# Optimization experiments

Measured on AMD Instinct MI355X. Metric: run time of the kernel, lower is better.

## Reference

```python
import jax, jax.numpy as jnp
import numpy as np

B, S, H, NH = 2, 2048, 1024, 16
HD = H // NH
BASE = 10000.0


def _rotate_half(x):
    x1, x2 = x[..., : x.shape[-1] // 2], x[..., x.shape[-1] // 2 :]
    return jnp.concatenate((-x2, x1), axis=-1)


def setup_inputs() -> dict:
    key = jax.random.key(0)
    ks = jax.random.split(key, 6)
    hidden_states = jax.random.normal(ks[0], (B, S, H), jnp.float32)
    scale = 0.02
    wq = jax.random.normal(ks[1], (H, H), jnp.float32) * scale
    wk = jax.random.normal(ks[2], (H, H), jnp.float32) * scale
    wv = jax.random.normal(ks[3], (H, H), jnp.float32) * scale
    wo = jax.random.normal(ks[4], (H, H), jnp.float32) * scale
    # additive causal mask, shape (B, 1, S, S): 0 on/below diagonal, large negative above
    neg = jnp.finfo(jnp.float32).min
    causal = jnp.where(jnp.tril(jnp.ones((S, S), dtype=bool)), 0.0, neg).astype(jnp.float32)
    attention_mask = jnp.broadcast_to(causal[None, None], (B, 1, S, S))
    position_ids = jnp.broadcast_to(jnp.arange(S, dtype=jnp.int32)[None], (B, S))
    return {
        "hidden_states": hidden_states,
        "attention_mask": attention_mask,
        "wq": wq,
        "wk": wk,
        "wv": wv,
        "wo": wo,
        "position_ids": position_ids,
    }


def reference(hidden_states, attention_mask, wq, wk, wv, wo, position_ids):
    b, s, h = hidden_states.shape
    dtype = hidden_states.dtype

    def proj(x, w):  # torch Linear: y = x @ w.T, then split heads -> (b, nh, s, hd)
        y = jnp.einsum("bsh,oh->bso", x, w)
        return y.reshape(b, s, NH, HD).transpose(0, 2, 1, 3)

    q = proj(hidden_states, wq)
    k = proj(hidden_states, wk)
    v = proj(hidden_states, wv)

    # rotary cache (computed in fp32 like torch), gathered by position_ids
    inv_freq = 1.0 / (BASE ** (jnp.arange(0, HD, 2, dtype=jnp.float32) / HD))
    t = jnp.arange(s, dtype=jnp.float32)
    freqs = jnp.outer(t, inv_freq)                  # (s, hd/2)
    emb = jnp.concatenate((freqs, freqs), axis=-1)  # (s, hd)
    pos = jnp.clip(position_ids, 0, s - 1)
    cos = jnp.cos(emb).astype(dtype)[pos][:, None]  # (b, 1, s, hd)
    sin = jnp.sin(emb).astype(dtype)[pos][:, None]

    q = q * cos + _rotate_half(q) * sin
    k = k * cos + _rotate_half(k) * sin

    scores = jnp.einsum("bhqd,bhkd->bhqk", q, k) / jnp.sqrt(jnp.asarray(HD, dtype))
    scores = scores + attention_mask
    attn = jax.nn.softmax(scores.astype(jnp.float32), axis=-1).astype(dtype)
    out = jnp.einsum("bhqk,bhkd->bhqd", attn, v)    # (b, nh, s, hd)
    out = out.transpose(0, 2, 1, 3).reshape(b, s, h)
    return jnp.einsum("bso,ho->bsh", out, wo)
```

## Files before the change

### kernel.cpp

```cpp
#include <hip/hip_runtime.h>
#include <cstdint>
#include <cstddef>

typedef unsigned short u16;
typedef __bf16 bf16x8 __attribute__((ext_vector_type(8)));
typedef float f32x4 __attribute__((ext_vector_type(4)));

constexpr int SEQ = 2048;
constexpr int HID = 1024;
constexpr int NHEAD = 16;
constexpr int HDIM = 64;

typedef __attribute__((address_space(1))) void gvoid;
typedef __attribute__((address_space(3))) void lvoid;

__device__ __forceinline__ u16 f2bf(float f) {
  union { float f; unsigned u; } v;
  v.f = f;
  unsigned r = v.u + 0x7fffu + ((v.u >> 16) & 1u);
  return (u16)(r >> 16);
}
__device__ __forceinline__ u16 f2bf_trunc(float f) {
  union { float f; unsigned u; } v;
  v.f = f;
  return (u16)(v.u >> 16);
}

__device__ __forceinline__ f32x4 mfma16(bf16x8 a, bf16x8 b, f32x4 c) {
  return __builtin_amdgcn_mfma_f32_16x16x32_bf16(a, b, c, 0, 0, 0);
}

__device__ __forceinline__ int detect_f32(const unsigned* __restrict__ hs) {
  unsigned w = hs[threadIdx.x & 63];
  u16 lo = (u16)(w & 0xffffu);
  int e = (lo >> 7) & 0xff;
  bool inr = (e >= 100 && e <= 154);
  unsigned long long m = __ballot(inr);
  return (__popcll(m) >= 48) ? 0 : 1;
}

__global__ __launch_bounds__(256) void cvt_kernel(
    const void* s0, const void* s1, const void* s2, const void* s3, const void* s4,
    u16* __restrict__ d0, u16* __restrict__ dW,
    float* __restrict__ cosb, float* __restrict__ sinb) {
  int b = blockIdx.x;
  if (b >= 4096) {
    int idx = (b - 4096) * 256 + threadIdx.x;
    int s = idx >> 5;
    int i = idx & 31;
    float inv_freq = expf(-(float)(2 * i) * (9.210340371976184f / 64.0f));
    float ang = (float)s * inv_freq;
    float c = cosf(ang), sn = sinf(ang);
    cosb[s * 64 + i]      = c;
    cosb[s * 64 + i + 32] = c;
    sinb[s * 64 + i]      = sn;
    sinb[s * 64 + i + 32] = sn;
    return;
  }
  const int is_f32 = detect_f32((const unsigned*)s0);
  const void* s; u16* d; long base;
  if (b < 2048) { s = s0; d = d0; base = (long)b * 2048; }
  else {
    int bb = b - 2048;
    int w = bb >> 9;
    base = (long)(bb & 511) * 2048;
    s = (w == 0) ? s1 : (w == 1) ? s2 : (w == 2) ? s3 : s4;
    d = dW + (long)w * 1048576;
  }
  long idx = base + (long)threadIdx.x * 8;
  if (is_f32) {
    const float* sf = (const float*)s;
    float4 a = *(const float4*)(sf + idx);
    float4 c = *(const float4*)(sf + idx + 4);
    ushort4 p0, p1;
    p0.x = f2bf(a.x); p0.y = f2bf(a.y); p0.z = f2bf(a.z); p0.w = f2bf(a.w);
    p1.x = f2bf(c.x); p1.y = f2bf(c.y); p1.z = f2bf(c.z); p1.w = f2bf(c.w);
    *(ushort4*)(d + idx) = p0;
    *(ushort4*)(d + idx + 4) = p1;
  } else {
    const u16* su = (const u16*)s;
    *(uint4*)(d + idx) = *(const uint4*)(su + idx);
  }
}

__device__ __forceinline__ void gemm_mainloop_128(
    const u16* __restrict__ Ag, const u16* __restrict__ Bg,
    int row0, int col0, f32x4 acc[4][4]) {
  __shared__ __align__(16) u16 As[128 * 64];
  __shared__ __align__(16) u16 Bs[128 * 64];
  const int t = threadIdx.x;
  const int lane = t & 63, wave = t >> 6;
  const int l15 = lane & 15, quad = lane >> 4;
  const int wm = wave >> 1, wn = wave & 1;
  const int cs = ((lane & 7) ^ ((lane >> 3) & 7)) * 8;
  const u16* aS = Ag + (size_t)(row0 + wave * 32 + (lane >> 3)) * 1024 + cs;
  const u16* bS = Bg + (size_t)(col0 + wave * 32 + (lane >> 3)) * 1024 + cs;
  const int swz0 = ((quad)     ^ (l15 & 7)) * 8;
  const int swz1 = ((4 + quad) ^ (l15 & 7)) * 8;

  for (int k0 = 0; k0 < 1024; k0 += 64) {
    __syncthreads();
#pragma unroll
    for (int j = 0; j < 4; j++) {
      __builtin_amdgcn_global_load_lds((gvoid*)(aS + k0 + j * 8192),
                                       (lvoid*)(As + wave * 2048 + j * 512), 16, 0, 0);
      __builtin_amdgcn_global_load_lds((gvoid*)(bS + k0 + j * 8192),
                                       (lvoid*)(Bs + wave * 2048 + j * 512), 16, 0, 0);
    }
    __syncthreads();
#pragma unroll
    for (int kk = 0; kk < 2; kk++) {
      const int sw = kk ? swz1 : swz0;
      bf16x8 af[4], bfr[4];
#pragma unroll
      for (int i = 0; i < 4; i++)
        af[i] = *(const bf16x8*)(As + (wm * 64 + i * 16 + l15) * 64 + sw);
#pragma unroll
      for (int j = 0; j < 4; j++)
        bfr[j] = *(const bf16x8*)(Bs + (wn * 64 + j * 16 + l15) * 64 + sw);
#pragma unroll
      for (int i = 0; i < 4; i++)
#pragma unroll
        for (int j = 0; j < 4; j++)
          acc[i][j] = mfma16(af[i], bfr[j], acc[i][j]);
    }
  }
}

__global__ __launch_bounds__(256) void qkv_kernel(
    const u16* __restrict__ X, const u16* __restrict__ Wcat,
    const int* __restrict__ pos_ids,
    const float* __restrict__ cosb, const float* __restrict__ sinb,
    u16* __restrict__ q_ws, u16* __restrict__ k_ws, u16* __restrict__ vt_ws) {
  const int row0 = blockIdx.x * 128;
  const int col0 = blockIdx.y * 128;
  const int z = col0 >> 10;
  f32x4 acc[4][4];
#pragma unroll
  for (int i = 0; i < 4; i++)
#pragma unroll
    for (int j = 0; j < 4; j++) acc[i][j] = f32x4{0.f, 0.f, 0.f, 0.f};

  gemm_mainloop_128(X, Wcat, row0, col0, acc);

  const int t = threadIdx.x;
  const int lane = t & 63, wave = t >> 6;
  const int l15 = lane & 15, quad = lane >> 4;
  const int wm = wave >> 1, wn = wave & 1;
  const int gr0 = row0 + wm * 64;
  const int gc0 = col0 + wn * 64;
  const int nh = (gc0 >> 6) & 15;
  const float qscale = (z == 0) ? 0.18033688011112042f : 1.0f;

  if (z < 2) {
    u16* dst = (z == 0) ? q_ws : k_ws;
#pragma unroll
    for (int i = 0; i < 4; i++) {
#pragma unroll
      for (int r = 0; r < 4; r++) {
        int m = gr0 + i * 16 + quad * 4 + r;
        int b = m >> 11, s = m & 2047;
        int p = pos_ids[m];
        p = min(max(p, 0), SEQ - 1);
#pragma unroll
        for (int j = 0; j < 4; j++) {
          int d = j * 16 + l15;
          float c = cosb[p * 64 + d];
          float sn = sinb[p * 64 + d];
          float v = acc[i][j][r];
          float partner = acc[i][j ^ 2][r];
          float rot = (j < 2) ? -partner : partner;
          float o = (v * c + rot * sn) * qscale;
          dst[((size_t)((b * NHEAD + nh) * SEQ + s) << 6) + d] = f2bf(o);
        }
      }
    }
  } else {
#pragma unroll
    for (int i = 0; i < 4; i++) {
      int m_base = gr0 + i * 16 + quad * 4;
      int b = m_base >> 11, s = m_base & 2047;
#pragma unroll
      for (int j = 0; j < 4; j++) {
        int d = j * 16 + l15;
        ushort4 pk;
        pk.x = f2bf(acc[i][j][0]);
        pk.y = f2bf(acc[i][j][1]);
        pk.z = f2bf(acc[i][j][2]);
        pk.w = f2bf(acc[i][j][3]);
        *(ushort4*)(vt_ws + ((size_t)((b * NHEAD + nh) * 64 + d)) * SEQ + s) = pk;
      }
    }
  }
}

__global__ __launch_bounds__(256) void attn_kernel(
    const u16* __restrict__ q_ws, const u16* __restrict__ k_ws,
    const u16* __restrict__ vt_ws, u16* __restrict__ attn_ws) {
  const int b = blockIdx.z;
  const int qt = b ? blockIdx.x : 15 - blockIdx.x;
  const int nh = blockIdx.y;
  const int bh = b * NHEAD + nh;
  __shared__ __align__(16) u16 Ks[128 * 64];
  __shared__ __align__(16) u16 Vts[64 * 128];
  __shared__ __align__(16) u16 Pl[128 * 64];

  const int t = threadIdx.x;
  const int lane = t & 63, wave = t >> 6;
  const int l15 = lane & 15, quad = lane >> 4;
  const int l7 = l15 & 7;
  const int wq0 = qt * 128 + wave * 32;

  bf16x8 aq[2][2];
#pragma unroll
  for (int i = 0; i < 2; i++) {
    const u16* qb = q_ws + ((size_t)bh * SEQ + wq0 + i * 16 + l15) * 64;
    aq[i][0] = *(const bf16x8*)(qb + quad * 8);
    aq[i][1] = *(const bf16x8*)(qb + 32 + quad * 8);
  }

  f32x4 O[2][4];
  float lp[2][4];
#pragma unroll
  for (int i = 0; i < 2; i++)
#pragma unroll
    for (int n = 0; n < 4; n++) { O[i][n] = f32x4{0.f, 0.f, 0.f, 0.f}; lp[i][n] = 0.f; }

  const int krl = lane >> 3;
  const int kcs = ((lane & 7) ^ (krl & 7)) * 8;
  const u16* kS = k_ws + (size_t)bh * SEQ * 64 + (size_t)(wave * 32 + krl) * 64 + kcs;
  const int vrl = lane >> 4;
  const int vc4 = lane & 15;
  const u16* vS = vt_ws + (size_t)bh * 64 * SEQ + (size_t)(wave * 16 + vrl) * SEQ;
  int vx[4];
#pragma unroll
  for (int j = 0; j < 4; j++) vx[j] = (vc4 ^ ((4 * j + vrl) & 15)) * 8;

  const int nkt = qt + 1;
  for (int kt = 0; kt < nkt; ++kt) {
    __syncthreads();
    const size_t koff = (size_t)kt * 8192;
#pragma unroll
    for (int j = 0; j < 4; j++) {
      __builtin_amdgcn_global_load_lds((gvoid*)(kS + koff + j * 512),
                                       (lvoid*)(Ks + wave * 2048 + j * 512), 16, 0, 0);
      __builtin_amdgcn_global_load_lds((gvoid*)(vS + (size_t)j * 4 * SEQ + kt * 128 + vx[j]),
                                       (lvoid*)(Vts + wave * 2048 + j * 512), 16, 0, 0);
    }
    __syncthreads();

#pragma unroll
    for (int h = 0; h < 2; h++) {
      f32x4 sc[2][4];
#pragma unroll
      for (int ct = 0; ct < 4; ct++) {
        const u16* krow = Ks + (h * 64 + ct * 16 + l15) * 64;
        bf16x8 bk0 = *(const bf16x8*)(krow + (quad ^ l7) * 8);
        bf16x8 bk1 = *(const bf16x8*)(krow + ((4 + quad) ^ l7) * 8);
#pragma unroll
        for (int i = 0; i < 2; i++) {
          f32x4 z = f32x4{0.f, 0.f, 0.f, 0.f};
          z = mfma16(aq[i][0], bk0, z);
          z = mfma16(aq[i][1], bk1, z);
          sc[i][ct] = z;
        }
      }

      if (kt == qt) {
#pragma unroll
        for (int i = 0; i < 2; i++) {
          const int qrow = wq0 + i * 16 + quad * 4;
#pragma unroll
          for (int ct = 0; ct < 4; ct++) {
            const int key = kt * 128 + h * 64 + ct * 16 + l15;
#pragma unroll
            for (int r = 0; r < 4; r++) {
              const int row = quad * 4 + r;
              float p = __builtin_amdgcn_exp2f(sc[i][ct][r]);
              if (key > qrow + r) p = 0.f;
              lp[i][r] += p;
              Pl[(wave * 32 + i * 16 + row) * 64 +
                 (((ct * 2 + (l15 >> 3)) ^ (row & 7)) * 8) + l7] = f2bf_trunc(p);
            }
          }
        }
      } else {
#pragma unroll
        for (int i = 0; i < 2; i++) {
#pragma unroll
          for (int ct = 0; ct < 4; ct++) {
#pragma unroll
            for (int r = 0; r < 4; r++) {
              const int row = quad * 4 + r;
              float p = __builtin_amdgcn_exp2f(sc[i][ct][r]);
              lp[i][r] += p;
              Pl[(wave * 32 + i * 16 + row) * 64 +
                 (((ct * 2 + (l15 >> 3)) ^ (row & 7)) * 8) + l7] = f2bf_trunc(p);
            }
          }
        }
      }

      bf16x8 pa[2][2];
#pragma unroll
      for (int i = 0; i < 2; i++) {
        const u16* prow = Pl + (wave * 32 + i * 16 + l15) * 64;
        pa[i][0] = *(const bf16x8*)(prow + (quad ^ l7) * 8);
        pa[i][1] = *(const bf16x8*)(prow + ((4 + quad) ^ l7) * 8);
      }
#pragma unroll
      for (int n = 0; n < 4; n++) {
        const u16* vrow = Vts + (n * 16 + l15) * 128;
        bf16x8 bv0 = *(const bf16x8*)(vrow + ((h * 8 + quad) ^ l15) * 8);
        bf16x8 bv1 = *(const bf16x8*)(vrow + ((h * 8 + 4 + quad) ^ l15) * 8);
#pragma unroll
        for (int i = 0; i < 2; i++) {
          O[i][n] = mfma16(pa[i][0], bv0, O[i][n]);
          O[i][n] = mfma16(pa[i][1], bv1, O[i][n]);
        }
      }
    }
  }

#pragma unroll
  for (int i = 0; i < 2; i++) {
#pragma unroll
    for (int r = 0; r < 4; r++) {
      float l = lp[i][r];
      l += __shfl_xor(l, 1, 64);
      l += __shfl_xor(l, 2, 64);
      l += __shfl_xor(l, 4, 64);
      l += __shfl_xor(l, 8, 64);
      float inv = 1.0f / l;
      int q = wq0 + i * 16 + quad * 4 + r;
      size_t base = ((size_t)(b * SEQ + q)) * HID + nh * 64;
#pragma unroll
      for (int n = 0; n < 4; n++)
        attn_ws[base + n * 16 + l15] = f2bf(O[i][n][r] * inv);
    }
  }
}

__global__ __launch_bounds__(256) void out_proj_kernel(
    const u16* __restrict__ A, const u16* __restrict__ Wo, void* __restrict__ out,
    const unsigned* __restrict__ hs_raw) {
  __shared__ __align__(16) u16 As[64 * 64];
  __shared__ __align__(16) u16 Bs[128 * 64];
  const int row0 = blockIdx.x * 64;
  const int col0 = blockIdx.y * 128;
  const int is_f32 = detect_f32(hs_raw);
  const int t = threadIdx.x;
  const int lane = t & 63, wave = t >> 6;
  const int l15 = lane & 15, quad = lane >> 4;
  const int wm = wave >> 1, wn = wave & 1;
  const int cs = ((lane & 7) ^ ((lane >> 3) & 7)) * 8;
  const u16* aS = A  + (size_t)(row0 + wave * 16 + (lane >> 3)) * 1024 + cs;
  const u16* bS = Wo + (size_t)(col0 + wave * 32 + (lane >> 3)) * 1024 + cs;
  const int swz0 = ((quad)     ^ (l15 & 7)) * 8;
  const int swz1 = ((4 + quad) ^ (l15 & 7)) * 8;

  f32x4 acc[2][4];
#pragma unroll
  for (int i = 0; i < 2; i++)
#pragma unroll
    for (int j = 0; j < 4; j++) acc[i][j] = f32x4{0.f, 0.f, 0.f, 0.f};

  for (int k0 = 0; k0 < 1024; k0 += 64) {
    __syncthreads();
#pragma unroll
    for (int j = 0; j < 2; j++)
      __builtin_amdgcn_global_load_lds((gvoid*)(aS + k0 + j * 8192),
                                       (lvoid*)(As + wave * 1024 + j * 512), 16, 0, 0);
#pragma unroll
    for (int j = 0; j < 4; j++)
      __builtin_amdgcn_global_load_lds((gvoid*)(bS + k0 + j * 8192),
                                       (lvoid*)(Bs + wave * 2048 + j * 512), 16, 0, 0);
    __syncthreads();
#pragma unroll
    for (int kk = 0; kk < 2; kk++) {
      const int sw = kk ? swz1 : swz0;
      bf16x8 af[2], bfr[4];
#pragma unroll
      for (int i = 0; i < 2; i++)
        af[i] = *(const bf16x8*)(As + (wm * 32 + i * 16 + l15) * 64 + sw);
#pragma unroll
      for (int j = 0; j < 4; j++)
        bfr[j] = *(const bf16x8*)(Bs + (wn * 64 + j * 16 + l15) * 64 + sw);
#pragma unroll
      for (int i = 0; i < 2; i++)
#pragma unroll
        for (int j = 0; j < 4; j++)
          acc[i][j] = mfma16(af[i], bfr[j], acc[i][j]);
    }
  }

  const int gr0 = row0 + wm * 32;
  const int gc0 = col0 + wn * 64;
#pragma unroll
  for (int i = 0; i < 2; i++)
#pragma unroll
    for (int r = 0; r < 4; r++) {
      int m = gr0 + i * 16 + quad * 4 + r;
      if (is_f32) {
        float* o = (float*)out;
#pragma unroll
        for (int j = 0; j < 4; j++)
          o[(size_t)m * 1024 + gc0 + j * 16 + l15] = acc[i][j][r];
      } else {
        u16* o = (u16*)out;
#pragma unroll
        for (int j = 0; j < 4; j++)
          o[(size_t)m * 1024 + gc0 + j * 16 + l15] = f2bf(acc[i][j][r]);
      }
    }
}

extern "C" void kernel_launch(void* const* d_in, const int* in_sizes, int n_in,
                              void* d_out, int out_size, void* d_ws, size_t ws_size,
                              hipStream_t stream) {
  const void* hs = d_in[0];
  const void* wq = d_in[2];
  const void* wk = d_in[3];
  const void* wv = d_in[4];
  const void* wo = d_in[5];
  const int* pos = (const int*)d_in[6];

  char* ws = (char*)d_ws;
  float* cosb = (float*)ws;
  float* sinb = (float*)(ws + (512 << 10));
  u16* xbf    = (u16*)(ws + (1 << 20));
  u16* wcat   = xbf + (size_t)4194304;
  u16* q_ws   = wcat + (size_t)4 * 1048576;
  u16* k_ws   = q_ws + (size_t)2 * NHEAD * SEQ * HDIM;
  u16* vt_ws  = k_ws + (size_t)2 * NHEAD * SEQ * HDIM;
  u16* attn_ws = vt_ws + (size_t)2 * NHEAD * SEQ * HDIM;

  cvt_kernel<<<4352, 256, 0, stream>>>(hs, wq, wk, wv, wo, xbf, wcat, cosb, sinb);
  qkv_kernel<<<dim3(32, 24), 256, 0, stream>>>(xbf, wcat, pos, cosb, sinb,
                                               q_ws, k_ws, vt_ws);
  attn_kernel<<<dim3(16, NHEAD, 2), 256, 0, stream>>>(q_ws, k_ws, vt_ws, attn_ws);
  out_proj_kernel<<<dim3(64, 8), 256, 0, stream>>>(attn_ws, wcat + (size_t)3 * 1048576,
                                                   d_out, (const unsigned*)hs);
}
```

Before: 201.3 us.

## Double-buffer K/V tiles in attention and transpose score MFMA for packed P stores

Adds a second LDS buffer for K and V^T so the next key tile is loaded asynchronously while the current tile is computed, using vmcnt waits and raw barriers instead of two syncthreads per iteration. Swaps the MFMA operand order for QK^T so each lane holds four consecutive keys of one query row. This lets P be written to LDS as packed 4-element stores and row sums be kept per lane, reduced with fewer shuffles. Also adds setprio hints around the MFMA blocks. The cost is more LDS per block, which can lower occupancy.

```diff
diff --git a/kernel.cpp b/kernel.cpp
--- a/kernel.cpp
+++ b/kernel.cpp
@@ -201,8 +201,8 @@
   const int qt = b ? blockIdx.x : 15 - blockIdx.x;
   const int nh = blockIdx.y;
   const int bh = b * NHEAD + nh;
-  __shared__ __align__(16) u16 Ks[128 * 64];
-  __shared__ __align__(16) u16 Vts[64 * 128];
+  __shared__ __align__(16) u16 Ks[2][128 * 64];
+  __shared__ __align__(16) u16 Vts[2][64 * 128];
   __shared__ __align__(16) u16 Pl[128 * 64];
 
   const int t = threadIdx.x;
@@ -220,11 +220,13 @@
   }
 
   f32x4 O[2][4];
-  float lp[2][4];
-#pragma unroll
-  for (int i = 0; i < 2; i++)
-#pragma unroll
-    for (int n = 0; n < 4; n++) { O[i][n] = f32x4{0.f, 0.f, 0.f, 0.f}; lp[i][n] = 0.f; }
+  float lp[2];
+#pragma unroll
+  for (int i = 0; i < 2; i++) {
+    lp[i] = 0.f;
+#pragma unroll
+    for (int n = 0; n < 4; n++) O[i][n] = f32x4{0.f, 0.f, 0.f, 0.f};
+  }
 
   const int krl = lane >> 3;
   const int kcs = ((lane & 7) ^ (krl & 7)) * 8;
@@ -236,67 +238,90 @@
 #pragma unroll
   for (int j = 0; j < 4; j++) vx[j] = (vc4 ^ ((4 * j + vrl) & 15)) * 8;
 
+#define STAGE_KV(bi, kt_) do {                                                     \
+    const size_t koff_ = (size_t)(kt_) * 8192;                                     \
+    _Pragma("unroll")                                                              \
+    for (int j = 0; j < 4; j++) {                                                  \
+      __builtin_amdgcn_global_load_lds((gvoid*)(kS + koff_ + j * 512),             \
+          (lvoid*)(&Ks[bi][0] + wave * 2048 + j * 512), 16, 0, 0);                 \
+      __builtin_amdgcn_global_load_lds(                                            \
+          (gvoid*)(vS + (size_t)j * 4 * SEQ + (kt_) * 128 + vx[j]),                \
+          (lvoid*)(&Vts[bi][0] + wave * 2048 + j * 512), 16, 0, 0);                \
+    }                                                                              \
+  } while (0)
+
   const int nkt = qt + 1;
+  STAGE_KV(0, 0);
+  int cur = 0;
   for (int kt = 0; kt < nkt; ++kt) {
-    __syncthreads();
-    const size_t koff = (size_t)kt * 8192;
-#pragma unroll
-    for (int j = 0; j < 4; j++) {
-      __builtin_amdgcn_global_load_lds((gvoid*)(kS + koff + j * 512),
-                                       (lvoid*)(Ks + wave * 2048 + j * 512), 16, 0, 0);
-      __builtin_amdgcn_global_load_lds((gvoid*)(vS + (size_t)j * 4 * SEQ + kt * 128 + vx[j]),
-                                       (lvoid*)(Vts + wave * 2048 + j * 512), 16, 0, 0);
-    }
-    __syncthreads();
+    if (kt + 1 < nkt) {
+      STAGE_KV(cur ^ 1, kt + 1);
+      asm volatile("s_waitcnt vmcnt(8)" ::: "memory");
+    } else {
+      asm volatile("s_waitcnt vmcnt(0)" ::: "memory");
+    }
+    __builtin_amdgcn_sched_barrier(0);
+    __builtin_amdgcn_s_barrier();
+    __builtin_amdgcn_sched_barrier(0);
+    const u16* Ksb = &Ks[cur][0];
+    const u16* Vtb = &Vts[cur][0];
 
 #pragma unroll
     for (int h = 0; h < 2; h++) {
       f32x4 sc[2][4];
+      __builtin_amdgcn_s_setprio(1);
 #pragma unroll
       for (int ct = 0; ct < 4; ct++) {
-        const u16* krow = Ks + (h * 64 + ct * 16 + l15) * 64;
+        const u16* krow = Ksb + (h * 64 + ct * 16 + l15) * 64;
         bf16x8 bk0 = *(const bf16x8*)(krow + (quad ^ l7) * 8);
         bf16x8 bk1 = *(const bf16x8*)(krow + ((4 + quad) ^ l7) * 8);
 #pragma unroll
         for (int i = 0; i < 2; i++) {
           f32x4 z = f32x4{0.f, 0.f, 0.f, 0.f};
-          z = mfma16(aq[i][0], bk0, z);
-          z = mfma16(aq[i][1], bk1, z);
+          z = mfma16(bk0, aq[i][0], z);
+          z = mfma16(bk1, aq[i][1], z);
           sc[i][ct] = z;
         }
       }
-
+      __builtin_amdgcn_s_setprio(0);
+
+      const int kbase = kt * 128 + h * 64;
       if (kt == qt) {
 #pragma unroll
         for (int i = 0; i < 2; i++) {
-          const int qrow = wq0 + i * 16 + quad * 4;
+          const int qrow = wq0 + i * 16 + l15;
+          const int prow = (wave * 32 + i * 16 + l15) * 64;
 #pragma unroll
           for (int ct = 0; ct < 4; ct++) {
-            const int key = kt * 128 + h * 64 + ct * 16 + l15;
+            const int key0 = kbase + ct * 16 + quad * 4;
+            float p[4];
 #pragma unroll
             for (int r = 0; r < 4; r++) {
-              const int row = quad * 4 + r;
-              float p = __builtin_amdgcn_exp2f(sc[i][ct][r]);
-              if (key > qrow + r) p = 0.f;
-              lp[i][r] += p;
-              Pl[(wave * 32 + i * 16 + row) * 64 +
-                 (((ct * 2 + (l15 >> 3)) ^ (row & 7)) * 8) + l7] = f2bf_trunc(p);
+              float e = __builtin_amdgcn_exp2f(sc[i][ct][r]);
+              if (key0 + r > qrow) e = 0.f;
+              p[r] = e;
             }
+            lp[i] += (p[0] + p[1]) + (p[2] + p[3]);
+            ushort4 pk;
+            pk.x = f2bf_trunc(p[0]); pk.y = f2bf_trunc(p[1]);
+            pk.z = f2bf_trunc(p[2]); pk.w = f2bf_trunc(p[3]);
+            *(ushort4*)&Pl[prow + ((ct * 2 + (quad >> 1)) ^ l7) * 8 + (quad & 1) * 4] = pk;
           }
         }
       } else {
 #pragma unroll
         for (int i = 0; i < 2; i++) {
+          const int prow = (wave * 32 + i * 16 + l15) * 64;
 #pragma unroll
           for (int ct = 0; ct < 4; ct++) {
-#pragma unroll
-            for (int r = 0; r < 4; r++) {
-              const int row = quad * 4 + r;
-              float p = __builtin_amdgcn_exp2f(sc[i][ct][r]);
-              lp[i][r] += p;
-              Pl[(wave * 32 + i * 16 + row) * 64 +
-                 (((ct * 2 + (l15 >> 3)) ^ (row & 7)) * 8) + l7] = f2bf_trunc(p);
-            }
+            float p[4];
+#pragma unroll
+            for (int r = 0; r < 4; r++) p[r] = __builtin_amdgcn_exp2f(sc[i][ct][r]);
+            lp[i] += (p[0] + p[1]) + (p[2] + p[3]);
+            ushort4 pk;
+            pk.x = f2bf_trunc(p[0]); pk.y = f2bf_trunc(p[1]);
+            pk.z = f2bf_trunc(p[2]); pk.w = f2bf_trunc(p[3]);
+            *(ushort4*)&Pl[prow + ((ct * 2 + (quad >> 1)) ^ l7) * 8 + (quad & 1) * 4] = pk;
           }
         }
       }
@@ -308,9 +333,10 @@
         pa[i][0] = *(const bf16x8*)(prow + (quad ^ l7) * 8);
         pa[i][1] = *(const bf16x8*)(prow + ((4 + quad) ^ l7) * 8);
       }
+      __builtin_amdgcn_s_setprio(1);
 #pragma unroll
       for (int n = 0; n < 4; n++) {
-        const u16* vrow = Vts + (n * 16 + l15) * 128;
+        const u16* vrow = Vtb + (n * 16 + l15) * 128;
         bf16x8 bv0 = *(const bf16x8*)(vrow + ((h * 8 + quad) ^ l15) * 8);
         bf16x8 bv1 = *(const bf16x8*)(vrow + ((h * 8 + 4 + quad) ^ l15) * 8);
 #pragma unroll
@@ -319,19 +345,24 @@
           O[i][n] = mfma16(pa[i][1], bv1, O[i][n]);
         }
       }
-    }
-  }
+      __builtin_amdgcn_s_setprio(0);
+    }
+
+    __builtin_amdgcn_sched_barrier(0);
+    __builtin_amdgcn_s_barrier();
+    __builtin_amdgcn_sched_barrier(0);
+    cur ^= 1;
+  }
+#undef STAGE_KV
 
 #pragma unroll
   for (int i = 0; i < 2; i++) {
+    float l = lp[i];
+    l += __shfl_xor(l, 16, 64);
+    l += __shfl_xor(l, 32, 64);
 #pragma unroll
     for (int r = 0; r < 4; r++) {
-      float l = lp[i][r];
-      l += __shfl_xor(l, 1, 64);
-      l += __shfl_xor(l, 2, 64);
-      l += __shfl_xor(l, 4, 64);
-      l += __shfl_xor(l, 8, 64);
-      float inv = 1.0f / l;
+      float inv = 1.0f / __shfl(l, quad * 4 + r, 64);
       int q = wq0 + i * 16 + quad * 4 + r;
       size_t base = ((size_t)(b * SEQ + q)) * HID + nh * 64;
 #pragma unroll
```

Result: faster. 196.2 us (-2.5%).
